# Performance work log

Hardware: AMD Instinct MI355X
Metric: run time of the kernel (lower is better)

## Reference

```python
import jax, jax.numpy as jnp
import numpy as np

OBS_RADIUS = 1.0
N = 8192      # num_agents
IN_DIM = 4    # state dim: [x, y, vx, vy]
HID = 64


def setup_inputs() -> dict:
    key = jax.random.key(0)
    ks = jax.random.split(key, 6)
    states = jax.random.normal(ks[0], (N, IN_DIM), dtype=jnp.float32)
    W1 = jax.random.normal(ks[1], (IN_DIM, HID), dtype=jnp.float32) / np.sqrt(IN_DIM).astype(np.float32)
    b1 = jnp.zeros((HID,), jnp.float32)
    W2 = jax.random.normal(ks[2], (HID, HID), dtype=jnp.float32) / np.sqrt(HID).astype(np.float32)
    b2 = jnp.zeros((HID,), jnp.float32)
    cw = jax.random.normal(ks[3], (HID,), dtype=jnp.float32) / np.sqrt(HID).astype(np.float32)  # Conv1d(64,1,1) weight
    cb = jnp.zeros((1,), jnp.float32)
    return {"states": states, "W1": W1, "b1": b1, "W2": W2, "b2": b2, "cw": cw, "cb": cb}


def _build_norm_adj(states):
    # radius graph on first two coords (positions); no self edges in the edge list,
    # GCNConv then adds self-loops and does symmetric D^-1/2 (A+I) D^-1/2 normalization.
    pos = states[:, :2]
    d2 = jnp.sum((pos[:, None, :] - pos[None, :, :]) ** 2, axis=-1)  # [N, N]
    mask = d2 <= jnp.asarray(OBS_RADIUS ** 2, states.dtype)          # [N, N] bool (incl. diagonal)
    eye = jnp.eye(N, dtype=bool)
    A_hat = jnp.where(mask & ~eye, jnp.asarray(1.0, states.dtype), 0.0) + jnp.eye(N, dtype=states.dtype)
    dinv = jax.lax.rsqrt(jnp.sum(A_hat, axis=1))                     # deg >= 1 (self loop)
    A_norm = dinv[:, None] * A_hat * dinv[None, :]
    return A_norm, mask


def reference(states, W1, b1, W2, b2, cw, cb):
    A_norm, mask = _build_norm_adj(states)
    # GCNConv 1: aggregate(normalized adj) of X W, plus bias, ReLU
    h = jax.nn.relu(A_norm @ (states @ W1) + b1)   # [N, 64]
    # GCNConv 2
    h = jax.nn.relu(A_norm @ (h @ W2) + b2)        # [N, 64]
    # Conv1d(64 -> 1, kernel=1): pointwise linear over channels
    out = h @ cw[:, None] + cb                     # [N, 1]
    return out, mask
```

## Files before the change

### kernel.cpp

```cpp
#include <hip/hip_runtime.h>
#include <hip/hip_bf16.h>
#include <stdint.h>

#define NPTS 8192
#define MSTRIDE 260

typedef float f32x4 __attribute__((ext_vector_type(4)));
typedef short s16x8 __attribute__((ext_vector_type(8)));

__device__ __forceinline__ unsigned short f2bf(float f) {
    unsigned int u = __builtin_bit_cast(unsigned int, f);
    u += 0x7FFFu + ((u >> 16) & 1u);
    return (unsigned short)(u >> 16);
}


__global__ __launch_bounds__(256) void k_mask(const float* __restrict__ states,
                                              const float* __restrict__ W1,
                                              float* __restrict__ mout,
                                              unsigned long long* __restrict__ maskb,
                                              float* __restrict__ dinv,
                                              uint4* __restrict__ y1) {
    __shared__ float xs[NPTS];
    __shared__ float ys[NPTS];
    __shared__ float dls[16];
    int tid = threadIdx.x;
    for (int r = tid; r < NPTS; r += 256) {
        float4 s = ((const float4*)states)[r];
        xs[r] = s.x; ys[r] = s.y;
    }
    __syncthreads();
    int wv = tid >> 6, L = tid & 63;
    int rowbase = blockIdx.x * 16 + wv * 4;
    float xi[4], yi[4];
    int deg[4] = {0, 0, 0, 0};
#pragma unroll
    for (int rr = 0; rr < 4; ++rr) { xi[rr] = xs[rowbase + rr]; yi[rr] = ys[rowbase + rr]; }
    for (int it = 0; it < 128; ++it) {
        int j = it * 64 + L;
        float xj = xs[j], yj = ys[j];
#pragma unroll
        for (int rr = 0; rr < 4; ++rr) {
            float dx = xi[rr] - xj;
            float dy = yi[rr] - yj;
            float d2 = __fadd_rn(__fmul_rn(dx, dx), __fmul_rn(dy, dy));
            bool pred = (d2 <= 1.0f);
            __builtin_nontemporal_store(pred ? 1.0f : 0.0f,
                                        &mout[(size_t)(rowbase + rr) * NPTS + j]);
            unsigned long long b = __ballot(pred);
            if (L == 0) maskb[(size_t)(rowbase + rr) * 128 + it] = b;
            deg[rr] += (int)__popcll(b);
        }
    }
    if (L == 0) {
#pragma unroll
        for (int rr = 0; rr < 4; ++rr) {
            float dv = rsqrtf((float)deg[rr]);
            dinv[rowbase + rr] = dv;
            dls[wv * 4 + rr] = dv;
        }
    }
    __syncthreads();
    if (tid < 128) {
        int ql = tid >> 6;
        int ct = (tid >> 4) & 3;
        int nn = tid & 15;
        int col = ct * 16 + nn;
        float w0 = W1[col], w1 = W1[64 + col], w2 = W1[128 + col], w3 = W1[192 + col];
        unsigned short frag[8];
#pragma unroll
        for (int t = 0; t < 8; ++t) {
            int rloc = ql * 8 + t;
            int k = blockIdx.x * 16 + rloc;
            float4 s = ((const float4*)states)[k];
            float acc = s.x * w0 + s.y * w1 + s.z * w2 + s.w * w3;
            frag[t] = f2bf(dls[rloc] * acc);
        }
        uint4 u;
        u.x = (unsigned)frag[0] | ((unsigned)frag[1] << 16);
        u.y = (unsigned)frag[2] | ((unsigned)frag[3] << 16);
        u.z = (unsigned)frag[4] | ((unsigned)frag[5] << 16);
        u.w = (unsigned)frag[6] | ((unsigned)frag[7] << 16);
        int kb = blockIdx.x >> 1;
        int quad = ql + 2 * (blockIdx.x & 1);
        y1[(kb * 4 + ct) * 64 + quad * 16 + nn] = u;
    }
}

__device__ __forceinline__ void agg_core(const uint4* __restrict__ y,
                                         const unsigned int* __restrict__ maskb,
                                         const float* __restrict__ dinv,
                                         const float* __restrict__ bias,
                                         float* __restrict__ redbuf,
                                         unsigned int* __restrict__ mlds,
                                         float* __restrict__ hbuf,
                                         int R0) {
    int tid = threadIdx.x;
    {
        const uint4* src = (const uint4*)(maskb + (size_t)R0 * 256);
        for (int e = tid; e < 2048; e += 512) {
            uint4 v = src[e];
            int r = e >> 6, c4 = e & 63;
            *(uint4*)(mlds + r * MSTRIDE + c4 * 4) = v;
        }
    }
    __syncthreads();
    int w = tid >> 6, L = tid & 63;
    int n = L & 15, quad = L >> 4;
    const unsigned int* mr0 = mlds + n * MSTRIDE + w * 32;
    const unsigned int* mr1 = mr0 + 16 * MSTRIDE;
    const uint4* yb = y + (size_t)w * 8192 + L;

    f32x4 acc[2][4] = {{{0,0,0,0},{0,0,0,0},{0,0,0,0},{0,0,0,0}},
                       {{0,0,0,0},{0,0,0,0},{0,0,0,0},{0,0,0,0}}};
    uint4 b0[4], b1[4];
#pragma unroll
    for (int ct = 0; ct < 4; ++ct) b0[ct] = yb[ct * 64];
#pragma unroll
    for (int ct = 0; ct < 4; ++ct) b1[ct] = yb[256 + ct * 64];

    for (int kk = 0; kk < 32; kk += 2) {
        uint4 bn[4];
        if (kk + 2 < 32) {
            const uint4* p = yb + (kk + 2) * 256;
#pragma unroll
            for (int ct = 0; ct < 4; ++ct) bn[ct] = p[ct * 64];
        }
        {
            unsigned int mw0 = mr0[kk], mw1 = mr1[kk];
            unsigned int by0 = (mw0 >> (quad * 8)) & 0xFFu;
            unsigned int by1 = (mw1 >> (quad * 8)) & 0xFFu;
            s16x8 a0, a1;
#pragma unroll
            for (int t = 0; t < 8; ++t) {
                a0[t] = (short)(((by0 >> t) & 1u) ? 0x3F80 : 0);
                a1[t] = (short)(((by1 >> t) & 1u) ? 0x3F80 : 0);
            }
#pragma unroll
            for (int ct = 0; ct < 4; ++ct) {
                s16x8 b = __builtin_bit_cast(s16x8, b0[ct]);
                acc[0][ct] = __builtin_amdgcn_mfma_f32_16x16x32_bf16(a0, b, acc[0][ct], 0, 0, 0);
                acc[1][ct] = __builtin_amdgcn_mfma_f32_16x16x32_bf16(a1, b, acc[1][ct], 0, 0, 0);
            }
        }
#pragma unroll
        for (int ct = 0; ct < 4; ++ct) b0[ct] = bn[ct];
        if (kk + 3 < 32) {
            const uint4* p = yb + (kk + 3) * 256;
#pragma unroll
            for (int ct = 0; ct < 4; ++ct) bn[ct] = p[ct * 64];
        }
        {
            unsigned int mw0 = mr0[kk + 1], mw1 = mr1[kk + 1];
            unsigned int by0 = (mw0 >> (quad * 8)) & 0xFFu;
            unsigned int by1 = (mw1 >> (quad * 8)) & 0xFFu;
            s16x8 a0, a1;
#pragma unroll
            for (int t = 0; t < 8; ++t) {
                a0[t] = (short)(((by0 >> t) & 1u) ? 0x3F80 : 0);
                a1[t] = (short)(((by1 >> t) & 1u) ? 0x3F80 : 0);
            }
#pragma unroll
            for (int ct = 0; ct < 4; ++ct) {
                s16x8 b = __builtin_bit_cast(s16x8, b1[ct]);
                acc[0][ct] = __builtin_amdgcn_mfma_f32_16x16x32_bf16(a0, b, acc[0][ct], 0, 0, 0);
                acc[1][ct] = __builtin_amdgcn_mfma_f32_16x16x32_bf16(a1, b, acc[1][ct], 0, 0, 0);
            }
        }
#pragma unroll
        for (int ct = 0; ct < 4; ++ct) b1[ct] = bn[ct];
    }
    float* rb = redbuf + w * 2048;
#pragma unroll
    for (int g = 0; g < 2; ++g)
#pragma unroll
        for (int ct = 0; ct < 4; ++ct)
#pragma unroll
            for (int r = 0; r < 4; ++r)
                rb[(g * 16 + quad * 4 + r) * 64 + ct * 16 + n] = acc[g][ct][r];
    __syncthreads();
    for (int e = tid; e < 2048; e += 512) {
        float z = 0.0f;
#pragma unroll
        for (int ww = 0; ww < 8; ++ww) z += redbuf[ww * 2048 + e];
        int row = e >> 6, col = e & 63;
        hbuf[row * 66 + col] = fmaxf(dinv[R0 + row] * z + bias[col], 0.0f);
    }
    __syncthreads();
}

__global__ __launch_bounds__(512) void k_layer1(const uint4* __restrict__ y1,
                                                const unsigned int* __restrict__ maskb,
                                                const float* __restrict__ dinv,
                                                const float* __restrict__ b1,
                                                const float* __restrict__ W2,
                                                uint4* __restrict__ y2) {
    __shared__ float redbuf[8 * 2048];
    __shared__ unsigned int mlds[32 * MSTRIDE];
    __shared__ float hbuf[32 * 66];
    __shared__ float w2s[4096];
    int tid = threadIdx.x;
    for (int s = tid; s < 4096; s += 512) w2s[s] = W2[s];
    int R0 = blockIdx.x * 32;
    agg_core(y1, maskb, dinv, b1, redbuf, mlds, hbuf, R0);
    {
        int nn = tid & 15, q = (tid >> 4) & 3, ct = (tid >> 6) & 3, half = tid >> 8;
        int col = ct * 16 + nn;
        float dot[4] = {0, 0, 0, 0};
        for (int m = 0; m < 64; ++m) {
            float wv = w2s[m * 64 + col];
#pragma unroll
            for (int t = 0; t < 4; ++t)
                dot[t] = fmaf(hbuf[(q * 8 + half * 4 + t) * 66 + m], wv, dot[t]);
        }
        unsigned short v[4];
#pragma unroll
        for (int t = 0; t < 4; ++t) v[t] = f2bf(dinv[R0 + q * 8 + half * 4 + t] * dot[t]);
        uint2 u;
        u.x = (unsigned)v[0] | ((unsigned)v[1] << 16);
        u.y = (unsigned)v[2] | ((unsigned)v[3] << 16);
        int fragidx = (blockIdx.x * 4 + ct) * 64 + q * 16 + nn;
        ((uint2*)y2)[fragidx * 2 + half] = u;
    }
}

__global__ __launch_bounds__(512) void k_layer2(const uint4* __restrict__ y2,
                                                const unsigned int* __restrict__ maskb,
                                                const float* __restrict__ dinv,
                                                const float* __restrict__ b2,
                                                const float* __restrict__ cw,
                                                const float* __restrict__ cb,
                                                float* __restrict__ out) {
    __shared__ float redbuf[8 * 2048];
    __shared__ unsigned int mlds[32 * MSTRIDE];
    __shared__ float hbuf[32 * 66];
    __shared__ float cws[64];
    int tid = threadIdx.x;
    if (tid < 64) cws[tid] = cw[tid];
    int R0 = blockIdx.x * 32;
    agg_core(y2, maskb, dinv, b2, redbuf, mlds, hbuf, R0);
    int row = tid >> 4, cg = tid & 15;
    float v = 0.0f;
#pragma unroll
    for (int e = 0; e < 4; ++e) {
        int c = cg * 4 + e;
        v = fmaf(hbuf[row * 66 + c], cws[c], v);
    }
    v += __shfl_down(v, 8);
    v += __shfl_down(v, 4);
    v += __shfl_down(v, 2);
    v += __shfl_down(v, 1);
    if (cg == 0) out[R0 + row] = v + cb[0];
}

extern "C" void kernel_launch(void* const* d_in, const int* in_sizes, int n_in,
                              void* d_out, int out_size, void* d_ws, size_t ws_size,
                              hipStream_t stream) {
    const float* states = (const float*)d_in[0];
    const float* W1 = (const float*)d_in[1];
    const float* b1 = (const float*)d_in[2];
    const float* W2 = (const float*)d_in[3];
    const float* b2 = (const float*)d_in[4];
    const float* cw = (const float*)d_in[5];
    const float* cb = (const float*)d_in[6];
    float* out = (float*)d_out;
    float* mout = out + NPTS;

    char* ws = (char*)d_ws;
    float* dinv               = (float*)(ws);
    unsigned long long* maskb = (unsigned long long*)(ws + (1 << 16));
    uint4* y1                 = (uint4*)(ws + (1 << 16) + (8 << 20));
    uint4* y2                 = (uint4*)(ws + (1 << 16) + (9 << 20));

    hipLaunchKernelGGL(k_mask,   dim3(512), dim3(256), 0, stream,
                       states, W1, mout, maskb, dinv, y1);
    hipLaunchKernelGGL(k_layer1, dim3(256), dim3(512), 0, stream,
                       y1, (const unsigned int*)maskb, dinv, b1, W2, y2);
    hipLaunchKernelGGL(k_layer2, dim3(256), dim3(512), 0, stream,
                       y2, (const unsigned int*)maskb, dinv, b2, cw, cb, out);
}
```

Baseline: 334.7 us.

## Stage mask bits in LDS, emit vectorized mask stores, triple-buffer aggregation loads

The mask kernel now keeps ballot bitmasks in shared memory instead of writing a scalar float per lane per row. It then writes the float mask with 16-byte nontemporal vector stores expanded from those bits, and copies the bitmask to global with coalesced uint4 stores. In the aggregation kernel the double-buffered B prefetch becomes a fully unrolled triple-buffered ring, with the next mask word prefetched one step ahead. These changes target the store-bound mask output and load latency in the MFMA loop, at the cost of extra LDS use and a separate expansion pass.

```diff
diff --git a/kernel.cpp b/kernel.cpp
--- a/kernel.cpp
+++ b/kernel.cpp
@@ -23,6 +23,7 @@
                                               uint4* __restrict__ y1) {
     __shared__ float xs[NPTS];
     __shared__ float ys[NPTS];
+    __shared__ unsigned long long mbits[16 * 128];
     __shared__ float dls[16];
     int tid = threadIdx.x;
     for (int r = tid; r < NPTS; r += 256) {
@@ -32,35 +33,50 @@
     __syncthreads();
     int wv = tid >> 6, L = tid & 63;
     int rowbase = blockIdx.x * 16 + wv * 4;
-    float xi[4], yi[4];
-    int deg[4] = {0, 0, 0, 0};
-#pragma unroll
-    for (int rr = 0; rr < 4; ++rr) { xi[rr] = xs[rowbase + rr]; yi[rr] = ys[rowbase + rr]; }
-    for (int it = 0; it < 128; ++it) {
-        int j = it * 64 + L;
-        float xj = xs[j], yj = ys[j];
-#pragma unroll
-        for (int rr = 0; rr < 4; ++rr) {
-            float dx = xi[rr] - xj;
-            float dy = yi[rr] - yj;
+#pragma unroll
+    for (int rr = 0; rr < 4; ++rr) {
+        int row = wv * 4 + rr;
+        float xi = xs[rowbase + rr], yi = ys[rowbase + rr];
+        int deg = 0;
+        for (int it = 0; it < 128; ++it) {
+            int j = it * 64 + L;
+            float dx = xi - xs[j];
+            float dy = yi - ys[j];
             float d2 = __fadd_rn(__fmul_rn(dx, dx), __fmul_rn(dy, dy));
             bool pred = (d2 <= 1.0f);
-            __builtin_nontemporal_store(pred ? 1.0f : 0.0f,
-                                        &mout[(size_t)(rowbase + rr) * NPTS + j]);
             unsigned long long b = __ballot(pred);
-            if (L == 0) maskb[(size_t)(rowbase + rr) * 128 + it] = b;
-            deg[rr] += (int)__popcll(b);
-        }
-    }
-    if (L == 0) {
-#pragma unroll
-        for (int rr = 0; rr < 4; ++rr) {
-            float dv = rsqrtf((float)deg[rr]);
+            if (L == 0) mbits[row * 128 + it] = b;
+            deg += (int)__popcll(b);
+        }
+        if (L == 0) {
+            float dv = rsqrtf((float)deg);
             dinv[rowbase + rr] = dv;
-            dls[wv * 4 + rr] = dv;
-        }
-    }
-    __syncthreads();
+            dls[row] = dv;
+        }
+    }
+    __syncthreads();
+    {
+        const uint4* s = (const uint4*)mbits;
+        uint4* d = (uint4*)(maskb + (size_t)blockIdx.x * 16 * 128);
+        for (int e = tid; e < 1024; e += 256) d[e] = s[e];
+    }
+#pragma unroll
+    for (int rr = 0; rr < 4; ++rr) {
+        int row = wv * 4 + rr;
+        const unsigned long long* mr = mbits + row * 128;
+        float* orow = mout + (size_t)(rowbase + rr) * NPTS;
+        int wsel = L >> 4, bsel = (L & 15) * 4;
+        for (int it2 = 0; it2 < 32; ++it2) {
+            unsigned long long word = mr[it2 * 4 + wsel];
+            unsigned int nib = (unsigned int)(word >> bsel) & 0xFu;
+            f32x4 v;
+            v.x = (float)(nib & 1u);
+            v.y = (float)((nib >> 1) & 1u);
+            v.z = (float)((nib >> 2) & 1u);
+            v.w = (float)((nib >> 3) & 1u);
+            __builtin_nontemporal_store(v, (f32x4*)(orow + it2 * 256 + L * 4));
+        }
+    }
     if (tid < 128) {
         int ql = tid >> 6;
         int ct = (tid >> 4) & 3;
@@ -113,62 +129,38 @@
 
     f32x4 acc[2][4] = {{{0,0,0,0},{0,0,0,0},{0,0,0,0},{0,0,0,0}},
                        {{0,0,0,0},{0,0,0,0},{0,0,0,0},{0,0,0,0}}};
-    uint4 b0[4], b1[4];
-#pragma unroll
-    for (int ct = 0; ct < 4; ++ct) b0[ct] = yb[ct * 64];
-#pragma unroll
-    for (int ct = 0; ct < 4; ++ct) b1[ct] = yb[256 + ct * 64];
-
-    for (int kk = 0; kk < 32; kk += 2) {
-        uint4 bn[4];
-        if (kk + 2 < 32) {
-            const uint4* p = yb + (kk + 2) * 256;
-#pragma unroll
-            for (int ct = 0; ct < 4; ++ct) bn[ct] = p[ct * 64];
-        }
-        {
-            unsigned int mw0 = mr0[kk], mw1 = mr1[kk];
-            unsigned int by0 = (mw0 >> (quad * 8)) & 0xFFu;
-            unsigned int by1 = (mw1 >> (quad * 8)) & 0xFFu;
-            s16x8 a0, a1;
-#pragma unroll
-            for (int t = 0; t < 8; ++t) {
-                a0[t] = (short)(((by0 >> t) & 1u) ? 0x3F80 : 0);
-                a1[t] = (short)(((by1 >> t) & 1u) ? 0x3F80 : 0);
-            }
-#pragma unroll
-            for (int ct = 0; ct < 4; ++ct) {
-                s16x8 b = __builtin_bit_cast(s16x8, b0[ct]);
-                acc[0][ct] = __builtin_amdgcn_mfma_f32_16x16x32_bf16(a0, b, acc[0][ct], 0, 0, 0);
-                acc[1][ct] = __builtin_amdgcn_mfma_f32_16x16x32_bf16(a1, b, acc[1][ct], 0, 0, 0);
-            }
-        }
-#pragma unroll
-        for (int ct = 0; ct < 4; ++ct) b0[ct] = bn[ct];
+    uint4 B[3][4];
+#pragma unroll
+    for (int s = 0; s < 3; ++s)
+#pragma unroll
+        for (int ct = 0; ct < 4; ++ct) B[s][ct] = yb[s * 256 + ct * 64];
+    unsigned int mw0 = mr0[0], mw1 = mr1[0];
+
+#pragma unroll
+    for (int kk = 0; kk < 32; ++kk) {
+        int cur = kk % 3;
+        unsigned int mwn0 = 0, mwn1 = 0;
+        if (kk + 1 < 32) { mwn0 = mr0[kk + 1]; mwn1 = mr1[kk + 1]; }
+        unsigned int by0 = (mw0 >> (quad * 8)) & 0xFFu;
+        unsigned int by1 = (mw1 >> (quad * 8)) & 0xFFu;
+        s16x8 a0, a1;
+#pragma unroll
+        for (int t = 0; t < 8; ++t) {
+            a0[t] = (short)(((by0 >> t) & 1u) ? 0x3F80 : 0);
+            a1[t] = (short)(((by1 >> t) & 1u) ? 0x3F80 : 0);
+        }
+#pragma unroll
+        for (int ct = 0; ct < 4; ++ct) {
+            s16x8 b = __builtin_bit_cast(s16x8, B[cur][ct]);
+            acc[0][ct] = __builtin_amdgcn_mfma_f32_16x16x32_bf16(a0, b, acc[0][ct], 0, 0, 0);
+            acc[1][ct] = __builtin_amdgcn_mfma_f32_16x16x32_bf16(a1, b, acc[1][ct], 0, 0, 0);
+        }
         if (kk + 3 < 32) {
             const uint4* p = yb + (kk + 3) * 256;
 #pragma unroll
-            for (int ct = 0; ct < 4; ++ct) bn[ct] = p[ct * 64];
-        }
-        {
-            unsigned int mw0 = mr0[kk + 1], mw1 = mr1[kk + 1];
-            unsigned int by0 = (mw0 >> (quad * 8)) & 0xFFu;
-            unsigned int by1 = (mw1 >> (quad * 8)) & 0xFFu;
-            s16x8 a0, a1;
-#pragma unroll
-            for (int t = 0; t < 8; ++t) {
-                a0[t] = (short)(((by0 >> t) & 1u) ? 0x3F80 : 0);
-                a1[t] = (short)(((by1 >> t) & 1u) ? 0x3F80 : 0);
-            }
-#pragma unroll
-            for (int ct = 0; ct < 4; ++ct) {
-                s16x8 b = __builtin_bit_cast(s16x8, b1[ct]);
-                acc[0][ct] = __builtin_amdgcn_mfma_f32_16x16x32_bf16(a0, b, acc[0][ct], 0, 0, 0);
-                acc[1][ct] = __builtin_amdgcn_mfma_f32_16x16x32_bf16(a1, b, acc[1][ct], 0, 0, 0);
-            }
-        }
-#pragma unroll
-        for (int ct = 0; ct < 4; ++ct) b1[ct] = bn[ct];
+            for (int ct = 0; ct < 4; ++ct) B[cur][ct] = p[ct * 64];
+        }
+        mw0 = mwn0; mw1 = mwn1;
     }
     float* rb = redbuf + w * 2048;
 #pragma unroll
```

New measurement: 391.7 us. +17.1%, slower.
